# Performance work log

Hardware: AMD Instinct MI355X
Metric: run time of the kernel (lower is better)

Reference implementation:

```python
import jax, jax.numpy as jnp
import numpy as np

B, C, H, W = 16, 1024, 32, 32  # H*W must equal C (required by matmul(h, fg) in the source)
EPS = 1e-5
NEG_SLOPE = 0.01


def setup_inputs() -> dict:
    key = jax.random.key(0)
    ks = jax.random.split(key, 12)
    s = 1.0 / np.sqrt(C)
    inp = {"x": jax.random.normal(ks[0], (B, C, H, W), jnp.float32)}
    for i, name in enumerate(["f", "g", "h", "c"]):
        inp[f"W{name}"] = jax.random.normal(ks[1 + 2 * i], (C, C), jnp.float32) * s
        inp[f"b{name}"] = jax.random.normal(ks[2 + 2 * i], (C,), jnp.float32) * 0.01
    inp["gamma"] = jnp.ones((C,), jnp.float32)
    inp["beta"] = jnp.zeros((C,), jnp.float32)
    inp["rmean"] = jax.random.normal(ks[9], (C,), jnp.float32) * 0.01
    inp["rvar"] = jax.random.uniform(ks[10], (C,), jnp.float32, 0.5, 1.5)
    return inp


def reference(x, Wf, bf, Wg, bg, Wh, bh, Wc, bc, gamma, beta, rmean, rvar):
    b, c, h_, w_ = x.shape
    n = h_ * w_  # == c by construction
    xf = x.reshape(b, c, n)

    def proj(Wp, bp):  # 1x1 conv == per-pixel channel matmul
        return jnp.einsum('oc,bcn->bon', Wp, xf) + bp[None, :, None]

    f = proj(Wf, bf)              # (B, C, N)
    g = proj(Wg, bg)              # (B, C, N); transposed(1,2) handled in einsum
    hh = proj(Wh, bh)             # (B, C, N)
    scores = jnp.einsum('bcn,bdn->bcd', f, g)        # f @ g^T -> (B, C, C)
    attn = jax.nn.softmax(scores, axis=1)            # softmax over dim=1 (as in source)
    # dropout2d(p=0.5) is identity in eval mode
    hfg = jnp.einsum('bcn,bnd->bcd', hh, attn)       # matmul(h, fg), needs N == C
    hfg = hfg.reshape(b, c, h_, w_)
    y = jnp.einsum('oc,bchw->bohw', Wc, hfg) + bc[None, :, None, None]
    y = jnp.where(y >= 0, y, NEG_SLOPE * y)          # LeakyReLU
    inv = gamma / jnp.sqrt(rvar + EPS)               # BatchNorm (eval mode)
    y = (y - rmean[None, :, None, None]) * inv[None, :, None, None] + beta[None, :, None, None]
    return y + x
```

## Files before the change

kernel.cpp:

```cpp
#include <hip/hip_runtime.h>
#include <cstdint>
#include <cstddef>

using half8  = __attribute__((ext_vector_type(8))) _Float16;
using half4  = __attribute__((ext_vector_type(4))) _Float16;
using float4v = __attribute__((ext_vector_type(4))) float;

#define CD 1024
#define M2 (1024 * 1024)

#define GLD16(gp, lp)                                                          \
    __builtin_amdgcn_global_load_lds(                                          \
        (const __attribute__((address_space(1))) void*)(gp),                   \
        (__attribute__((address_space(3))) void*)(lp), 16, 0, 0)

__global__ void prep_weights(const float* __restrict__ Wf, const float* __restrict__ Wg,
                             const float* __restrict__ Wh, const float* __restrict__ Wc,
                             const float* __restrict__ bf, const float* __restrict__ bg,
                             const float* __restrict__ bh,
                             _Float16* __restrict__ Wfgh, _Float16* __restrict__ WcH,
                             float* __restrict__ bstack) {
    int idx = blockIdx.x * 256 + threadIdx.x;
    if (idx < 3 * M2) {
        const float* s = idx < M2 ? Wf : (idx < 2 * M2 ? Wg : Wh);
        int off = idx & (M2 - 1);
        Wfgh[idx] = (_Float16)s[off];
    } else if (idx < 4 * M2) {
        WcH[idx - 3 * M2] = (_Float16)Wc[idx - 3 * M2];
    } else if (idx < 4 * M2 + 3 * CD) {
        int j = idx - 4 * M2;
        const float* s = j < CD ? bf : (j < 2 * CD ? bg : bh);
        bstack[j] = s[j & (CD - 1)];
    }
}

__global__ void transpose_x(const float* __restrict__ x, _Float16* __restrict__ xT, int b0) {
    __shared__ float tile[32][33];
    int z = blockIdx.z;
    const float* xb = x + (size_t)(b0 + z) * M2;
    _Float16* xTb = xT + (size_t)z * M2;
    int n0 = blockIdx.x * 32, k0 = blockIdx.y * 32;
    int tx = threadIdx.x, ty = threadIdx.y;
#pragma unroll
    for (int i = 0; i < 4; i++)
        tile[ty + i * 8][tx] = xb[(size_t)(k0 + ty + i * 8) * CD + n0 + tx];
    __syncthreads();
#pragma unroll
    for (int i = 0; i < 4; i++)
        xTb[(size_t)(n0 + ty + i * 8) * CD + k0 + tx] = (_Float16)tile[tx][ty + i * 8];
}

__global__ __launch_bounds__(256) void softmax_col(const float* __restrict__ ST,
                                                   _Float16* __restrict__ attnT) {
    int d = blockIdx.x, z = blockIdx.y;
    const float* row = ST + ((size_t)z * CD + d) * CD;
    _Float16* orow = attnT + ((size_t)z * CD + d) * CD;
    int t = threadIdx.x;
    float4v v = *(const float4v*)(row + t * 4);
    float mx = fmaxf(fmaxf(v[0], v[1]), fmaxf(v[2], v[3]));
#pragma unroll
    for (int o = 32; o > 0; o >>= 1) mx = fmaxf(mx, __shfl_xor(mx, o));
    __shared__ float redm[4], reds[4];
    int wave = t >> 6, lane = t & 63;
    if (lane == 0) redm[wave] = mx;
    __syncthreads();
    mx = fmaxf(fmaxf(redm[0], redm[1]), fmaxf(redm[2], redm[3]));
    float e[4];
    float s = 0.f;
#pragma unroll
    for (int i = 0; i < 4; i++) {
        e[i] = __expf(v[i] - mx);
        s += e[i];
    }
#pragma unroll
    for (int o = 32; o > 0; o >>= 1) s += __shfl_xor(s, o);
    if (lane == 0) reds[wave] = s;
    __syncthreads();
    s = reds[0] + reds[1] + reds[2] + reds[3];
    float inv = 1.0f / s;
    half4 ov;
#pragma unroll
    for (int i = 0; i < 4; i++) ov[i] = (_Float16)(e[i] * inv);
    *(half4*)(orow + t * 4) = ov;
}

enum { EP_F16B = 0, EP_F32 = 1, EP_F16 = 2, EP_FIN = 3 };

#define STAGE_A(T, BUF)                                                        \
    GLD16(gA0 + (size_t)(T) * 32, &As[BUF][wv * 16][0]);                       \
    GLD16(gA1 + (size_t)(T) * 32, &As[BUF][128 + wv * 16][0]);
#define STAGE_B(T, BUF)                                                        \
    GLD16(gB0 + (size_t)(T) * 32, &Bs[BUF][wv * 16][0]);                       \
    GLD16(gB1 + (size_t)(T) * 32, &Bs[BUF][128 + wv * 16][0]);

#define TILE(BUF, DOSTAGE, STT, STBUF, VMSTR)                                  \
    {                                                                          \
        asm volatile("s_waitcnt " VMSTR ::: "memory");                         \
        __builtin_amdgcn_sched_barrier(0);                                     \
        __builtin_amdgcn_s_barrier();                                          \
        _Pragma("unroll") for (int m = 0; m < 4; m++)                          \
            a[m] = *(const half8*)&As[BUF][wr * 128 + m * 16 + rl][kqa];       \
        _Pragma("unroll") for (int n = 0; n < 4; n++)                          \
            b[n] = *(const half8*)&Bs[BUF][wc * 64 + n * 16 + rl][kqa];        \
        _Pragma("unroll") for (int m = 4; m < 8; m++)                          \
            a[m] = *(const half8*)&As[BUF][wr * 128 + m * 16 + rl][kqa];       \
        if (DOSTAGE) { STAGE_A(STT, STBUF) STAGE_B(STT, STBUF) }               \
        __builtin_amdgcn_sched_barrier(0);                                     \
        __builtin_amdgcn_s_setprio(1);                                         \
        _Pragma("unroll") for (int m = 0; m < 8; m++)                          \
            _Pragma("unroll") for (int n = 0; n < 4; n++)                      \
                acc[m][n] = __builtin_amdgcn_mfma_f32_16x16x32_f16(            \
                    a[m], b[n], acc[m][n], 0, 0, 0);                           \
        __builtin_amdgcn_s_setprio(0);                                         \
    }

template <int EPI>
__global__ __launch_bounds__(512, 2) void gemm_nt(
    const _Float16* __restrict__ A, int64_t sA, const _Float16* __restrict__ B, int64_t sB,
    void* __restrict__ Cp, int64_t sC, const float* __restrict__ bias,
    const float* __restrict__ bc, const float* __restrict__ gamma,
    const float* __restrict__ beta, const float* __restrict__ rmean,
    const float* __restrict__ rvar, const float* __restrict__ xres) {
    __shared__ __align__(16) _Float16 As[4][256][32];
    __shared__ __align__(16) _Float16 Bs[4][256][32];
    int z = blockIdx.z;
    const _Float16* Ab = A + (size_t)z * sA;
    const _Float16* Bb = B + (size_t)z * sB;
    int row0 = blockIdx.y * 256, col0 = blockIdx.x * 256;
    int tid = threadIdx.x, lane = tid & 63, wv = tid >> 6;
    int wr = wv >> 2, wc = wv & 3;

    const int srow = wv * 16 + (lane >> 2);
    const int scol = ((lane & 3) ^ ((lane >> 3) & 3)) * 8;
    const _Float16* gA0 = Ab + (size_t)(row0 + srow) * 1024 + scol;
    const _Float16* gA1 = gA0 + (size_t)128 * 1024;
    const _Float16* gB0 = Bb + (size_t)(col0 + srow) * 1024 + scol;
    const _Float16* gB1 = gB0 + (size_t)128 * 1024;

    const int rl = lane & 15;
    const int kq = (lane >> 4) * 8;
    const int kqa = kq ^ (((rl >> 1) & 3) << 3);

    float4v acc[8][4] = {};
    half8 a[8], b[4];

    STAGE_A(0, 0) STAGE_B(0, 0)
    STAGE_A(1, 1) STAGE_B(1, 1)
    STAGE_A(2, 2) STAGE_B(2, 2)

#pragma unroll 1
    for (int g = 0; g < 7; ++g) {
        int t = g * 4;
        TILE(0, 1, t + 3, 3, "vmcnt(8)")
        TILE(1, 1, t + 4, 0, "vmcnt(8)")
        TILE(2, 1, t + 5, 1, "vmcnt(8)")
        TILE(3, 1, t + 6, 2, "vmcnt(8)")
    }
    TILE(0, 1, 31, 3, "vmcnt(8)")
    TILE(1, 0, 0, 0, "vmcnt(8)")
    TILE(2, 0, 0, 0, "vmcnt(4)")
    TILE(3, 0, 0, 0, "vmcnt(0)")

#pragma unroll
    for (int m = 0; m < 8; m++) {
#pragma unroll
        for (int r = 0; r < 4; r++) {
            int row = row0 + wr * 128 + m * 16 + ((lane >> 4) << 2) + r;
            float add0 = 0.f, mu = 0.f, invs = 1.f, bet = 0.f;
            if constexpr (EPI == EP_F16B) add0 = bias[row];
            if constexpr (EPI == EP_FIN) {
                add0 = bc[row];
                mu = rmean[row];
                invs = gamma[row] * rsqrtf(rvar[row] + 1e-5f);
                bet = beta[row];
            }
#pragma unroll
            for (int n = 0; n < 4; n++) {
                int col = col0 + wc * 64 + n * 16 + (lane & 15);
                float v = acc[m][n][r];
                if constexpr (EPI == EP_F16B) {
                    ((_Float16*)Cp)[(size_t)z * sC + (size_t)row * 1024 + col] = (_Float16)(v + add0);
                } else if constexpr (EPI == EP_F32) {
                    ((float*)Cp)[(size_t)z * sC + (size_t)row * 1024 + col] = v;
                } else if constexpr (EPI == EP_F16) {
                    ((_Float16*)Cp)[(size_t)z * sC + (size_t)row * 1024 + col] = (_Float16)v;
                } else {
                    v += add0;
                    v = v >= 0.f ? v : 0.01f * v;
                    v = (v - mu) * invs + bet;
                    v += xres[(size_t)z * M2 + (size_t)row * 1024 + col];
                    ((float*)Cp)[(size_t)z * sC + (size_t)row * 1024 + col] = v;
                }
            }
        }
    }
}

extern "C" void kernel_launch(void* const* d_in, const int* in_sizes, int n_in,
                              void* d_out, int out_size, void* d_ws, size_t ws_size,
                              hipStream_t stream) {
    const float* x = (const float*)d_in[0];
    const float* Wf = (const float*)d_in[1];
    const float* bf = (const float*)d_in[2];
    const float* Wg = (const float*)d_in[3];
    const float* bg = (const float*)d_in[4];
    const float* Wh = (const float*)d_in[5];
    const float* bh = (const float*)d_in[6];
    const float* Wc = (const float*)d_in[7];
    const float* bc = (const float*)d_in[8];
    const float* gamma = (const float*)d_in[9];
    const float* beta = (const float*)d_in[10];
    const float* rmean = (const float*)d_in[11];
    const float* rvar = (const float*)d_in[12];

    char* p = (char*)d_ws;
    _Float16* Wfgh = (_Float16*)p;
    p += (size_t)3 * M2 * 2;
    _Float16* WcH = (_Float16*)p;
    p += (size_t)M2 * 2;
    float* bstack = (float*)p;
    p += (size_t)3 * CD * 4;
    size_t fixed = (size_t)(p - (char*)d_ws);
    fixed = (fixed + 255) & ~(size_t)255;

    size_t perB = (size_t)2 * M2 + (size_t)6 * M2 + (size_t)4 * M2;
    int nb = 16;
    while (nb > 1 && fixed + (size_t)nb * perB > ws_size) nb >>= 1;

    {
        int total = 4 * M2 + 3 * CD;
        prep_weights<<<dim3((total + 255) / 256), dim3(256), 0, stream>>>(
            Wf, Wg, Wh, Wc, bf, bg, bh, Wfgh, WcH, bstack);
    }

    for (int b0 = 0; b0 < 16; b0 += nb) {
        char* q = (char*)d_ws + fixed;
        _Float16* xT = (_Float16*)q;
        _Float16* FGH = (_Float16*)(q + (size_t)nb * 2 * M2);
        float* ST = (float*)(q + (size_t)nb * 8 * M2);
        _Float16* attnT = xT;
        _Float16* hfgT = (_Float16*)ST;

        transpose_x<<<dim3(32, 32, nb), dim3(32, 8), 0, stream>>>(x, xT, b0);
        gemm_nt<EP_F16B><<<dim3(4, 12, nb), dim3(512), 0, stream>>>(
            Wfgh, 0, xT, M2, FGH, (int64_t)3 * M2, bstack,
            nullptr, nullptr, nullptr, nullptr, nullptr, nullptr);
        gemm_nt<EP_F32><<<dim3(4, 4, nb), dim3(512), 0, stream>>>(
            FGH + M2, (int64_t)3 * M2, FGH, (int64_t)3 * M2, ST, M2,
            nullptr, nullptr, nullptr, nullptr, nullptr, nullptr, nullptr);
        softmax_col<<<dim3(1024, nb), dim3(256), 0, stream>>>(ST, attnT);
        gemm_nt<EP_F16><<<dim3(4, 4, nb), dim3(512), 0, stream>>>(
            attnT, M2, FGH + 2 * M2, (int64_t)3 * M2, hfgT, M2,
            nullptr, nullptr, nullptr, nullptr, nullptr, nullptr, nullptr);
        gemm_nt<EP_FIN><<<dim3(4, 4, nb), dim3(512), 0, stream>>>(
            WcH, 0, hfgT, M2, (float*)d_out + (size_t)b0 * M2, M2,
            nullptr, bc, gamma, beta, rmean, rvar, x + (size_t)b0 * M2);
    }
}
```

Measured before the change: 301.3 us.

## Double-buffer LDS fragment registers to overlap LDS reads with MFMA

Restructures the GEMM main loop so LDS reads for the next k-tile go into a second register set while MFMAs run on the current set. The wait counts and barrier placement change so the global-to-LDS stage, barrier and next reads all come before the MFMA block. This is meant to hide LDS read latency behind matrix-core work. The cost is doubled fragment registers (48 more VGPRs), which could cause spills under launch_bounds(512,2), and a tighter vmcnt that may add stalls.

```diff
diff --git a/kernel.cpp b/kernel.cpp
--- a/kernel.cpp
+++ b/kernel.cpp
@@ -93,25 +93,30 @@
     GLD16(gB0 + (size_t)(T) * 32, &Bs[BUF][wv * 16][0]);                       \
     GLD16(gB1 + (size_t)(T) * 32, &Bs[BUF][128 + wv * 16][0]);
 
-#define TILE(BUF, DOSTAGE, STT, STBUF, VMSTR)                                  \
+#define READS(SET, BUF)                                                        \
+    _Pragma("unroll") for (int m = 0; m < 8; m++)                              \
+        a##SET[m] = *(const half8*)&As[BUF][wr * 128 + m * 16 + rl][kqa];      \
+    _Pragma("unroll") for (int n = 0; n < 4; n++)                              \
+        b##SET[n] = *(const half8*)&Bs[BUF][wc * 64 + n * 16 + rl][kqa];
+
+#define MFMA32(SET)                                                            \
+    __builtin_amdgcn_s_setprio(1);                                             \
+    _Pragma("unroll") for (int m = 0; m < 8; m++)                              \
+        _Pragma("unroll") for (int n = 0; n < 4; n++)                          \
+            acc[m][n] = __builtin_amdgcn_mfma_f32_16x16x32_f16(                \
+                a##SET[m], b##SET[n], acc[m][n], 0, 0, 0);                     \
+    __builtin_amdgcn_s_setprio(0);
+
+#define ITER(SETC, SETN, RBUF, DOSTAGE, STT, STBUF, DOVM, VMSTR, DOREAD, DOBAR)\
     {                                                                          \
-        asm volatile("s_waitcnt " VMSTR ::: "memory");                         \
-        __builtin_amdgcn_sched_barrier(0);                                     \
-        __builtin_amdgcn_s_barrier();                                          \
-        _Pragma("unroll") for (int m = 0; m < 4; m++)                          \
-            a[m] = *(const half8*)&As[BUF][wr * 128 + m * 16 + rl][kqa];       \
-        _Pragma("unroll") for (int n = 0; n < 4; n++)                          \
-            b[n] = *(const half8*)&Bs[BUF][wc * 64 + n * 16 + rl][kqa];        \
-        _Pragma("unroll") for (int m = 4; m < 8; m++)                          \
-            a[m] = *(const half8*)&As[BUF][wr * 128 + m * 16 + rl][kqa];       \
+        if (DOVM) {                                                            \
+            asm volatile("s_waitcnt " VMSTR ::: "memory");                     \
+            __builtin_amdgcn_sched_barrier(0);                                 \
+        }                                                                      \
+        if (DOBAR) __builtin_amdgcn_s_barrier();                               \
         if (DOSTAGE) { STAGE_A(STT, STBUF) STAGE_B(STT, STBUF) }               \
-        __builtin_amdgcn_sched_barrier(0);                                     \
-        __builtin_amdgcn_s_setprio(1);                                         \
-        _Pragma("unroll") for (int m = 0; m < 8; m++)                          \
-            _Pragma("unroll") for (int n = 0; n < 4; n++)                      \
-                acc[m][n] = __builtin_amdgcn_mfma_f32_16x16x32_f16(            \
-                    a[m], b[n], acc[m][n], 0, 0, 0);                           \
-        __builtin_amdgcn_s_setprio(0);                                         \
+        if (DOREAD) { READS(SETN, RBUF) }                                      \
+        MFMA32(SETC)                                                           \
     }
 
 template <int EPI>
@@ -142,24 +147,28 @@
     const int kqa = kq ^ (((rl >> 1) & 3) << 3);
 
     float4v acc[8][4] = {};
-    half8 a[8], b[4];
+    half8 a0[8], b0[4], a1[8], b1[4];
 
     STAGE_A(0, 0) STAGE_B(0, 0)
     STAGE_A(1, 1) STAGE_B(1, 1)
     STAGE_A(2, 2) STAGE_B(2, 2)
+    asm volatile("s_waitcnt vmcnt(8)" ::: "memory");
+    __builtin_amdgcn_sched_barrier(0);
+    __builtin_amdgcn_s_barrier();
+    READS(0, 0)
 
 #pragma unroll 1
     for (int g = 0; g < 7; ++g) {
         int t = g * 4;
-        TILE(0, 1, t + 3, 3, "vmcnt(8)")
-        TILE(1, 1, t + 4, 0, "vmcnt(8)")
-        TILE(2, 1, t + 5, 1, "vmcnt(8)")
-        TILE(3, 1, t + 6, 2, "vmcnt(8)")
-    }
-    TILE(0, 1, 31, 3, "vmcnt(8)")
-    TILE(1, 0, 0, 0, "vmcnt(8)")
-    TILE(2, 0, 0, 0, "vmcnt(4)")
-    TILE(3, 0, 0, 0, "vmcnt(0)")
+        ITER(0, 1, 1, 1, t + 3, 3, 1, "vmcnt(4)", 1, 1)
+        ITER(1, 0, 2, 1, t + 4, 0, 1, "vmcnt(4)", 1, 1)
+        ITER(0, 1, 3, 1, t + 5, 1, 1, "vmcnt(4)", 1, 1)
+        ITER(1, 0, 0, 1, t + 6, 2, 1, "vmcnt(4)", 1, 1)
+    }
+    ITER(0, 1, 1, 1, 31, 3, 1, "vmcnt(4)", 1, 1)
+    ITER(1, 0, 2, 0, 0, 0, 1, "vmcnt(4)", 1, 1)
+    ITER(0, 1, 3, 0, 0, 0, 1, "vmcnt(0)", 1, 1)
+    ITER(1, 0, 0, 0, 0, 0, 0, "", 0, 0)
 
 #pragma unroll
     for (int m = 0; m < 8; m++) {
```

New measurement: 335.3 us. 1.11x slower.

## Fold Wc into Wh projection to eliminate one per-batch GEMM

Applied to the files above, without the earlier changes.

Precomputes Wc·Wh in fp16 and Wc·bh once, writes them into the h-projection slots, and computes the final output directly as (WcWh x + Wc bh)·attn. This exploits associativity to drop the separate h·attn GEMM and its intermediate buffer for every batch. It adds a small one-time weight GEMM and a gemv, and the combined weight is rounded to fp16, which may change numerical error slightly.

```diff
diff --git a/kernel.cpp b/kernel.cpp
--- a/kernel.cpp
+++ b/kernel.cpp
@@ -48,6 +48,69 @@
 #pragma unroll
     for (int i = 0; i < 4; i++)
         xTb[(size_t)(n0 + ty + i * 8) * CD + k0 + tx] = (_Float16)tile[tx][ty + i * 8];
+}
+
+__global__ __launch_bounds__(256) void gemv_bch(const float* __restrict__ Wc,
+                                                const float* __restrict__ bh,
+                                                float* __restrict__ bch) {
+    int o = blockIdx.x * 4 + (threadIdx.x >> 6);
+    int lane = threadIdx.x & 63;
+    float s = 0.f;
+    for (int c = lane; c < CD; c += 64) s += Wc[(size_t)o * CD + c] * bh[c];
+#pragma unroll
+    for (int off = 32; off > 0; off >>= 1) s += __shfl_xor(s, off);
+    if (lane == 0) bch[o] = s;
+}
+
+__global__ __launch_bounds__(256) void gemm128(const _Float16* __restrict__ A,
+                                               const _Float16* __restrict__ B,
+                                               _Float16* __restrict__ C) {
+    __shared__ __align__(16) _Float16 As[128][32];
+    __shared__ __align__(16) _Float16 Bs[128][32];
+    int row0 = blockIdx.y * 128, col0 = blockIdx.x * 128;
+    int tid = threadIdx.x, lane = tid & 63, wave = tid >> 6;
+    int wr = wave >> 1, wc = wave & 1;
+    const int srow = lane >> 2;
+    const int scol = (lane & 3) * 8;
+    const size_t gA0 = (size_t)(row0 + wave * 16 + srow) * 1024 + scol;
+    const size_t gA1 = gA0 + (size_t)64 * 1024;
+    const size_t gB0 = (size_t)(col0 + wave * 16 + srow) * 1024 + scol;
+    const size_t gB1 = gB0 + (size_t)64 * 1024;
+    _Float16* ldsA0 = &As[wave * 16][0];
+    _Float16* ldsA1 = &As[64 + wave * 16][0];
+    _Float16* ldsB0 = &Bs[wave * 16][0];
+    _Float16* ldsB1 = &Bs[64 + wave * 16][0];
+    float4v acc[4][4] = {};
+    const int kq = (lane >> 4) * 8, rl = lane & 15;
+    for (int kt = 0; kt < 1024; kt += 32) {
+        GLD16(A + gA0 + kt, ldsA0);
+        GLD16(A + gA1 + kt, ldsA1);
+        GLD16(B + gB0 + kt, ldsB0);
+        GLD16(B + gB1 + kt, ldsB1);
+        __syncthreads();
+        half8 af[4], bfr[4];
+#pragma unroll
+        for (int m = 0; m < 4; m++) af[m] = *(const half8*)(&As[wr * 64 + m * 16 + rl][kq]);
+#pragma unroll
+        for (int n = 0; n < 4; n++) bfr[n] = *(const half8*)(&Bs[wc * 64 + n * 16 + rl][kq]);
+#pragma unroll
+        for (int m = 0; m < 4; m++)
+#pragma unroll
+            for (int n = 0; n < 4; n++)
+                acc[m][n] = __builtin_amdgcn_mfma_f32_16x16x32_f16(af[m], bfr[n], acc[m][n], 0, 0, 0);
+        __syncthreads();
+    }
+#pragma unroll
+    for (int m = 0; m < 4; m++)
+#pragma unroll
+        for (int r = 0; r < 4; r++) {
+            int row = row0 + wr * 64 + m * 16 + ((lane >> 4) << 2) + r;
+#pragma unroll
+            for (int n = 0; n < 4; n++) {
+                int col = col0 + wc * 64 + n * 16 + (lane & 15);
+                C[(size_t)row * 1024 + col] = (_Float16)acc[m][n][r];
+            }
+        }
 }
 
 __global__ __launch_bounds__(256) void softmax_col(const float* __restrict__ ST,
@@ -227,19 +290,25 @@
     int nb = 16;
     while (nb > 1 && fixed + (size_t)nb * perB > ws_size) nb >>= 1;
 
+    char* q = (char*)d_ws + fixed;
+
     {
         int total = 4 * M2 + 3 * CD;
         prep_weights<<<dim3((total + 255) / 256), dim3(256), 0, stream>>>(
             Wf, Wg, Wh, Wc, bf, bg, bh, Wfgh, WcH, bstack);
     }
+    {
+        _Float16* WhT = (_Float16*)q;
+        transpose_x<<<dim3(32, 32, 1), dim3(32, 8), 0, stream>>>(Wh, WhT, 0);
+        gemv_bch<<<dim3(256), dim3(256), 0, stream>>>(Wc, bh, bstack + 2 * CD);
+        gemm128<<<dim3(8, 8), dim3(256), 0, stream>>>(WcH, WhT, Wfgh + (size_t)2 * M2);
+    }
 
     for (int b0 = 0; b0 < 16; b0 += nb) {
-        char* q = (char*)d_ws + fixed;
         _Float16* xT = (_Float16*)q;
         _Float16* FGH = (_Float16*)(q + (size_t)nb * 2 * M2);
         float* ST = (float*)(q + (size_t)nb * 8 * M2);
         _Float16* attnT = xT;
-        _Float16* hfgT = (_Float16*)ST;
 
         transpose_x<<<dim3(32, 32, nb), dim3(32, 8), 0, stream>>>(x, xT, b0);
         gemm_nt<EP_F16B><<<dim3(4, 12, nb), dim3(512), 0, stream>>>(
@@ -249,11 +318,9 @@
             FGH + M2, (int64_t)3 * M2, FGH, (int64_t)3 * M2, ST, M2,
             nullptr, nullptr, nullptr, nullptr, nullptr, nullptr, nullptr);
         softmax_col<<<dim3(1024, nb), dim3(256), 0, stream>>>(ST, attnT);
-        gemm_nt<EP_F16><<<dim3(4, 4, nb), dim3(512), 0, stream>>>(
-            attnT, M2, FGH + 2 * M2, (int64_t)3 * M2, hfgT, M2,
-            nullptr, nullptr, nullptr, nullptr, nullptr, nullptr, nullptr);
         gemm_nt<EP_FIN><<<dim3(4, 4, nb), dim3(512), 0, stream>>>(
-            WcH, 0, hfgT, M2, (float*)d_out + (size_t)b0 * M2, M2,
+            FGH + (size_t)2 * M2, (int64_t)3 * M2, attnT, M2,
+            (float*)d_out + (size_t)b0 * M2, M2,
             nullptr, bc, gamma, beta, rmean, rvar, x + (size_t)b0 * M2);
     }
 }
```

Result: faster. 290.7 us (-3.5%).
